# Performance work log

Measured on AMD Instinct MI355X. Metric: run time of the kernel, lower is better.

## Reference

```python
import jax, jax.numpy as jnp
import numpy as np
from jax import lax
jax.config.update("jax_enable_x64", True)

FNV_OFF = np.int64(-3750763034362895579)
FNV_PRIME = np.int64(4294967731)
I64_MAX = np.iinfo(np.int64).max
INF = np.float32(1e38)
CHUNK = 512  # cluster-chunk size for the cdist fallback


def _pack_key(b, c, vx, vy, vz):
    # five-word FNV-1a 64-bit hash with natural int64 wraparound
    h = jnp.full(b.shape, FNV_OFF, dtype=jnp.int64)
    for w in (b, c, vx, vy, vz):
        h = (h ^ w.astype(jnp.int64)) * FNV_PRIME
    return h


def _safe_norm(x):
    s = jnp.sum(x * x, axis=1)
    n = jnp.sqrt(jnp.where(s > 0, s, 1.0))
    return jnp.where(s > 0, n, 0.0)


def setup_inputs() -> dict:
    key = jax.random.key(0)
    k1, k2, k3, k4 = jax.random.split(key, 4)
    N = 65536
    grid = jax.random.randint(k1, (N, 3), 0, 400).astype(jnp.float32)
    batch_id = jnp.sort(jax.random.randint(k2, (N,), 0, 2).astype(jnp.int64))
    label = jax.random.randint(k3, (N,), 0, 8).astype(jnp.int64)
    pred_off = jax.random.normal(k4, (N, 3), dtype=jnp.float32)
    return {"pred_off": pred_off, "grid": grid, "label": label, "batch_id": batch_id,
            "base_grid": 16, "num_cls": 8, "num_batch": 2}


def _forward(pred_off, grid, label, batch_id, base_grid, num_cls, num_batch):
    N = grid.shape[0]
    grid_f = grid.astype(jnp.float32)
    vox = jnp.floor(grid_f / base_grid).astype(jnp.int64)  # [N,3]

    # voxel_grid: bucket by (batch, voxel) -> consecutive cluster ids via unique
    ckey = ((batch_id * 1024 + vox[:, 0]) * 1024 + vox[:, 1]) * 1024 + vox[:, 2]
    _, cluster = jnp.unique(ckey, return_inverse=True, size=N, fill_value=I64_MAX)
    cluster = cluster.reshape(-1)

    # cluster stats (segment scatter-reduce, num_segments = N upper bound)
    cnt = jax.ops.segment_sum(jnp.ones((N,), jnp.float32), cluster, num_segments=N)
    cl_center = jax.ops.segment_sum(grid_f, cluster, num_segments=N) / jnp.maximum(cnt, 1.0)[:, None]
    cl_batch = jax.ops.segment_min(batch_id, cluster, num_segments=N)
    cl_lbl_lo = jax.ops.segment_min(label, cluster, num_segments=N)
    cl_lbl_hi = jax.ops.segment_max(label, cluster, num_segments=N)
    cl_vox = jax.ops.segment_min(vox, cluster, num_segments=N)
    valid_cl = cnt > 0
    pure_cl = (cl_lbl_lo == cl_lbl_hi) & valid_cl
    pure_pt = pure_cl[cluster]

    # hash table of pure clusters, sorted by key (invalid -> sentinel, sorts last)
    pk_all = jnp.where(pure_cl, _pack_key(cl_batch, cl_lbl_lo, cl_vox[:, 0], cl_vox[:, 1], cl_vox[:, 2]), I64_MAX)
    order = jnp.argsort(pk_all)
    pk_sort = pk_all[order]
    pc_sort = cl_center[order]
    ok_sort = pure_cl[order]

    # per (batch,label) global centers
    key_bl = batch_id * num_cls + label
    nbl = num_batch * num_cls
    cnt_bl = jax.ops.segment_sum(jnp.ones((N,), jnp.float32), key_bl, num_segments=nbl)
    global_c = jax.ops.segment_sum(grid_f, key_bl, num_segments=nbl) / jnp.maximum(cnt_bl, 1.0)[:, None]
    step_sign = jnp.sign(global_c[key_bl] - cl_center[cluster]).astype(jnp.int64)  # [N,3]

    # +/-1 and +/-2 voxel hash lookup (steps 1 and K+1=2)
    def probe(step):
        cv = cl_vox[cluster] + step_sign * step
        ck = _pack_key(batch_id, label, cv[:, 0], cv[:, 1], cv[:, 2])
        idx = jnp.searchsorted(pk_sort, ck)
        idxc = jnp.minimum(idx, N - 1)
        hit = (idx < N) & ok_sort[idxc] & (pk_sort[idxc] == ck)
        return hit, pc_sort[idxc]

    hit1, t1 = probe(1)
    hit2, t2 = probe(2)
    hit_pt = hit1 | hit2
    tgt_c = jnp.where(hit1[:, None], t1, jnp.where(hit2[:, None], t2, grid_f))

    # fallback: nearest pure-cluster center with same (batch,label), chunked cdist+argmin
    miss = (~pure_pt) & (~hit_pt)
    code_y = key_bl
    code_x = jnp.where(pure_cl, cl_batch * num_cls + cl_lbl_lo, jnp.int64(-1))
    p2 = jnp.sum(grid_f * grid_f, axis=1)  # [N]

    def body(carry, i):
        best_d, best_c = carry
        c = lax.dynamic_slice_in_dim(cl_center, i * CHUNK, CHUNK)   # [S,3]
        cc = lax.dynamic_slice_in_dim(code_x, i * CHUNK, CHUNK)      # [S]
        d2 = p2[:, None] - 2.0 * (grid_f @ c.T) + jnp.sum(c * c, axis=1)[None, :]  # [N,S]
        d2 = jnp.where(cc[None, :] == code_y[:, None], d2, INF)
        j = jnp.argmin(d2, axis=1)
        dmin = jnp.take_along_axis(d2, j[:, None], axis=1)[:, 0]
        upd = dmin < best_d
        best_d = jnp.where(upd, dmin, best_d)
        best_c = jnp.where(upd[:, None], c[j], best_c)
        return (best_d, best_c), None

    nchunk = N // CHUNK
    (best_d, best_c), _ = lax.scan(body, (jnp.full((N,), INF, jnp.float32), grid_f), jnp.arange(nchunk))
    tgt_c = jnp.where((miss & (best_d < INF))[:, None], best_c, tgt_c)

    # loss: smooth-L1 on offsets below 99th-percentile magnitude + direction cosine loss
    tgt_off = tgt_c - grid_f
    mag = _safe_norm(tgt_off)
    thresh = jnp.quantile(mag, 0.99)
    m1 = mag <= thresh
    d = pred_off - tgt_off
    ad = jnp.abs(d)
    hub = jnp.where(ad < 1.0, 0.5 * d * d, ad - 0.5)
    n1 = jnp.sum(m1).astype(jnp.float32)
    loss_l1 = jnp.where(n1 > 0, jnp.sum(hub * m1[:, None]) / jnp.maximum(n1 * 3.0, 1.0), 0.0)

    md = (mag > 0) & m1
    eps = 1e-4
    pn = _safe_norm(pred_off)
    cos = jnp.sum(pred_off * tgt_off, axis=1) / jnp.maximum(pn * mag, eps)
    nmd = jnp.sum(md).astype(jnp.float32)
    loss_dir = jnp.where(nmd > 0, 1.0 - jnp.sum(cos * md) / jnp.maximum(nmd, 1.0), 0.0)
    return jnp.stack([loss_l1.astype(jnp.float32), loss_dir.astype(jnp.float32)])


def reference(pred_off, grid, label, batch_id, base_grid, num_cls, num_batch):
    return _forward(pred_off, grid, label, batch_id, base_grid, num_cls, num_batch)
```

## Files before the change

kernel.cpp:

```cpp
#include <hip/hip_runtime.h>
#include <climits>

#define VOXD 25
#define SLOT3 (VOXD*VOXD*VOXD)
#define SLOTS (2*SLOT3)
#define NCLS 8
#define NCODE 16
#define NBLK ((SLOTS + 255) / 256)
#define HB 2048
#define BPC 64
#define TILE 1024
#define CSTRIDE SLOT3

struct Scalars {
  double hub;
  double cosSum;
  int n1;
  int nmd;
  float thresh;
  int done;
  int done2;
};

__device__ __forceinline__ int voxslot(int b, int vx, int vy, int vz) {
  return ((b * VOXD + vx) * VOXD + vy) * VOXD + vz;
}

__device__ __forceinline__ int block_scan256(int v, int* ws) {
  int lane = threadIdx.x & 63, w = threadIdx.x >> 6;
  int s = v;
  #pragma unroll
  for (int off = 1; off < 64; off <<= 1) {
    int t = __shfl_up(s, off, 64);
    if (lane >= off) s += t;
  }
  if (lane == 63) ws[w] = s;
  __syncthreads();
  int add = 0;
  #pragma unroll
  for (int q = 0; q < 4; ++q) if (q < w) add += ws[q];
  __syncthreads();
  return s + add;
}

__global__ void k_scatter(const float* __restrict__ grid, const int* __restrict__ label,
                          const int* __restrict__ batch,
                          unsigned long long* vA, unsigned long long* vB, int* lmask,
                          int* blCnt, float* blSum, int n) {
  __shared__ int sCnt[NCODE];
  __shared__ float sSum[3 * NCODE];
  int tid = threadIdx.x;
  if (tid < NCODE) sCnt[tid] = 0;
  if (tid < 3 * NCODE) sSum[tid] = 0.f;
  __syncthreads();
  int i = blockIdx.x * blockDim.x + tid;
  if (i < n) {
    float gx = grid[3*i], gy = grid[3*i+1], gz = grid[3*i+2];
    int ix = (int)gx, iy = (int)gy, iz = (int)gz;
    int vx = (int)floorf(gx * (1.0f/16.0f));
    int vy = (int)floorf(gy * (1.0f/16.0f));
    int vz = (int)floorf(gz * (1.0f/16.0f));
    int b = batch[i], l = label[i];
    int s = voxslot(b, vx, vy, vz);
    atomicAdd(&vA[s], ((unsigned long long)(unsigned)ix << 32) | (unsigned)iy);
    atomicAdd(&vB[s], ((unsigned long long)(unsigned)iz << 24) | 1ULL);
    atomicOr(&lmask[s], 1 << l);
    int bl = b * NCLS + l;
    atomicAdd(&sCnt[bl], 1);
    atomicAdd(&sSum[3*bl], gx); atomicAdd(&sSum[3*bl+1], gy); atomicAdd(&sSum[3*bl+2], gz);
  }
  __syncthreads();
  if (tid < NCODE && sCnt[tid] != 0) atomicAdd(&blCnt[tid], sCnt[tid]);
  if (tid < 3 * NCODE && sSum[tid] != 0.f) atomicAdd(&blSum[tid], sSum[tid]);
}

__global__ void k_prep(const unsigned long long* vA, const unsigned long long* vB,
                       const int* lmask, float4* ctr, float4* pC, int* codeCnt) {
  __shared__ int lc[NCODE];
  __shared__ int lb[NCODE];
  int tid = threadIdx.x;
  if (tid < NCODE) lc[tid] = 0;
  __syncthreads();
  int s = blockIdx.x * 256 + tid;
  int code = -1, lpos = 0;
  float4 v = make_float4(0.f, 0.f, 0.f, __int_as_float(-2));
  if (s < SLOTS) {
    unsigned long long bq = vB[s];
    unsigned c = (unsigned)(bq & 0xFFFFFFULL);
    if (c > 0) {
      unsigned long long aq = vA[s];
      float fc = (float)c;
      float cx = __fdiv_rn((float)(unsigned)(aq >> 32), fc);
      float cy = __fdiv_rn((float)(unsigned)(aq & 0xFFFFFFFFULL), fc);
      float cz = __fdiv_rn((float)(unsigned)(bq >> 24), fc);
      int m = lmask[s];
      bool pure = (m & (m - 1)) == 0;
      int lbl = __ffs(m) - 1;
      v = make_float4(cx, cy, cz, __int_as_float(pure ? lbl : -1));
      if (pure) {
        code = (s / SLOT3) * NCLS + lbl;
        lpos = atomicAdd(&lc[code], 1);
      }
    }
    ctr[s] = v;
  }
  __syncthreads();
  if (tid < NCODE) lb[tid] = (lc[tid] > 0) ? atomicAdd(&codeCnt[tid], lc[tid]) : 0;
  __syncthreads();
  if (code >= 0) {
    int pos = code * CSTRIDE + lb[code] + lpos;
    pC[pos] = make_float4(v.x, v.y, v.z, __int_as_float(s));
  }
}

__global__ void k_targets(const float* __restrict__ grid, const int* __restrict__ label,
                          const int* __restrict__ batch,
                          const float4* __restrict__ ctr,
                          const int* __restrict__ blCnt, const float* __restrict__ blSum,
                          float* tgt, float* mag, int* ghist,
                          int* missPart, int* missCnt, int mstride, int n) {
  __shared__ int wCnt[4][NCODE];
  __shared__ int gBase[NCODE];
  __shared__ int h[HB];
  int tid = threadIdx.x, lane = tid & 63, w = tid >> 6;
  for (int t = tid; t < HB; t += 256) h[t] = 0;
  __syncthreads();
  int i = blockIdx.x * blockDim.x + tid;
  bool active = (i < n);
  bool miss = false;
  int mcode = -1;

  if (active) {
    float gx = grid[3*i], gy = grid[3*i+1], gz = grid[3*i+2];
    int vx = (int)floorf(gx * (1.0f/16.0f));
    int vy = (int)floorf(gy * (1.0f/16.0f));
    int vz = (int)floorf(gz * (1.0f/16.0f));
    int b = batch[i], l = label[i];
    int s = voxslot(b, vx, vy, vz);

    float4 own = ctr[s];
    bool purept = (__float_as_int(own.w) >= 0);

    int bl = b * NCLS + l;
    float fbc = (float)max(blCnt[bl], 1);
    float gcx = __fdiv_rn(blSum[3*bl],   fbc);
    float gcy = __fdiv_rn(blSum[3*bl+1], fbc);
    float gcz = __fdiv_rn(blSum[3*bl+2], fbc);

    float dx = __fsub_rn(gcx, own.x);
    float dy = __fsub_rn(gcy, own.y);
    float dz = __fsub_rn(gcz, own.z);
    int sgx = (dx > 0.f) ? 1 : ((dx < 0.f) ? -1 : 0);
    int sgy = (dy > 0.f) ? 1 : ((dy < 0.f) ? -1 : 0);
    int sgz = (dz > 0.f) ? 1 : ((dz < 0.f) ? -1 : 0);

    int ax1 = vx + sgx,     ay1 = vy + sgy,     az1 = vz + sgz;
    int ax2 = vx + 2 * sgx, ay2 = vy + 2 * sgy, az2 = vz + 2 * sgz;
    bool v1 = (unsigned)ax1 < (unsigned)VOXD && (unsigned)ay1 < (unsigned)VOXD &&
              (unsigned)az1 < (unsigned)VOXD;
    bool v2 = (unsigned)ax2 < (unsigned)VOXD && (unsigned)ay2 < (unsigned)VOXD &&
              (unsigned)az2 < (unsigned)VOXD;

    float4 q1 = make_float4(0.f, 0.f, 0.f, __int_as_float(-3));
    float4 q2 = q1;
    if (v1) q1 = ctr[voxslot(b, ax1, ay1, az1)];
    if (v2) q2 = ctr[voxslot(b, ax2, ay2, az2)];

    bool hit1 = v1 && (__float_as_int(q1.w) == l);
    bool hit2 = v2 && (__float_as_int(q2.w) == l);
    bool hit = hit1 || hit2;

    float tx = hit1 ? q1.x : (hit2 ? q2.x : gx);
    float ty = hit1 ? q1.y : (hit2 ? q2.y : gy);
    float tz = hit1 ? q1.z : (hit2 ? q2.z : gz);

    tgt[3*i] = tx; tgt[3*i+1] = ty; tgt[3*i+2] = tz;
    miss = (!purept && !hit);
    if (miss) {
      mcode = bl;
    } else {
      float tox = __fsub_rn(tx, gx), toy = __fsub_rn(ty, gy), toz = __fsub_rn(tz, gz);
      float ssq = __fadd_rn(__fadd_rn(__fmul_rn(tox,tox), __fmul_rn(toy,toy)),
                            __fmul_rn(toz,toz));
      float m = (ssq > 0.f) ? sqrtf(ssq) : 0.f;
      mag[i] = m;
      atomicAdd(&h[__float_as_uint(m) >> 21], 1);
    }
  }
  int myrank = 0;
  #pragma unroll
  for (int c = 0; c < NCODE; ++c) {
    unsigned long long mb = __ballot(mcode == c);
    if (lane == 0) wCnt[w][c] = __popcll(mb);
    if (mcode == c) myrank = __popcll(mb & ((1ULL << lane) - 1ULL));
  }
  __syncthreads();
  if (tid < NCODE) {
    int tot = wCnt[0][tid] + wCnt[1][tid] + wCnt[2][tid] + wCnt[3][tid];
    gBase[tid] = (tot > 0) ? atomicAdd(&missCnt[tid], tot) : 0;
  }
  __syncthreads();
  if (miss) {
    int base = gBase[mcode];
    for (int q = 0; q < 4; ++q) if (q < w) base += wCnt[q][mcode];
    missPart[mcode * mstride + base + myrank] = i;
  }
  for (int t = tid; t < HB; t += 256) {
    int c = h[t];
    if (c != 0) atomicAdd(&ghist[t], c);
  }
}

__global__ void __launch_bounds__(256) k_fallback(
    const float* __restrict__ grid,
    const float4* __restrict__ pC,
    const float4* __restrict__ ctr,
    const int* __restrict__ codeCnt,
    const int* __restrict__ missPart, const int* __restrict__ missCnt,
    float* tgt, float* mag, int* ghist, int mstride) {
  __shared__ float4 tile4[TILE];
  __shared__ int    stile[TILE];
  __shared__ unsigned long long bkeyw[4][64];
  __shared__ int h[HB];
  int tid = threadIdx.x, lane = tid & 63, w = tid >> 6;
  int c = blockIdx.x / BPC;
  int y = blockIdx.x % BPC;
  int mc = missCnt[c];
  if (y * 64 >= mc) return;
  int cc = codeCnt[c];
  int j0 = c * CSTRIDE;
  const int* mlist = missPart + c * mstride;

  for (int t = tid; t < HB; t += 256) h[t] = 0;
  __syncthreads();

  for (int t0 = y * 64; t0 < mc; t0 += BPC * 64) {
    int t = t0 + lane;
    bool valid = (t < mc);
    int idx = 0;
    float gx = 0.f, gy = 0.f, gz = 0.f, p2 = 0.f;
    if (valid) {
      idx = mlist[t];
      gx = grid[3*idx]; gy = grid[3*idx+1]; gz = grid[3*idx+2];
      p2 = __fadd_rn(__fadd_rn(__fmul_rn(gx,gx), __fmul_rn(gy,gy)),
                     __fmul_rn(gz,gz));
    }
    unsigned long long key = 0xFFFFFFFFFFFFFFFFULL;
    for (int tb = 0; tb < cc; tb += TILE) {
      int m = min(TILE, cc - tb);
      __syncthreads();
      for (int j = tid; j < m; j += 256) {
        float4 cl = pC[j0 + tb + j];
        float c2 = __fadd_rn(__fadd_rn(__fmul_rn(cl.x,cl.x), __fmul_rn(cl.y,cl.y)),
                             __fmul_rn(cl.z,cl.z));
        tile4[j] = make_float4(cl.x, cl.y, cl.z, c2);
        stile[j] = __float_as_int(cl.w);
      }
      __syncthreads();
      #pragma unroll 4
      for (int j = w; j < m; j += 4) {
        float4 cl = tile4[j];
        float dot = __fadd_rn(__fadd_rn(__fmul_rn(gx,cl.x), __fmul_rn(gy,cl.y)),
                              __fmul_rn(gz,cl.z));
        float d2 = __fadd_rn(__fsub_rn(p2, __fmul_rn(2.0f, dot)), cl.w);
        unsigned fb = __float_as_uint(d2);
        fb = (fb >> 31) ? ~fb : (fb | 0x80000000u);
        unsigned long long k2 = ((unsigned long long)fb << 32) | (unsigned)stile[j];
        if (k2 < key) key = k2;
      }
    }
    bkeyw[w][lane] = key;
    __syncthreads();
    if (w == 0 && valid) {
      unsigned long long k0 = bkeyw[0][lane];
      unsigned long long k1 = bkeyw[1][lane];
      unsigned long long k2_ = bkeyw[2][lane];
      unsigned long long k3 = bkeyw[3][lane];
      unsigned long long kk = k0 < k1 ? k0 : k1;
      unsigned long long kh = k2_ < k3 ? k2_ : k3;
      if (kh < kk) kk = kh;
      float mv = 0.f;
      if (cc > 0) {
        int slot = (int)(unsigned)(kk & 0xFFFFFFFFULL);
        float4 cl = ctr[slot];
        tgt[3*idx] = cl.x; tgt[3*idx+1] = cl.y; tgt[3*idx+2] = cl.z;
        float tox = __fsub_rn(cl.x, gx), toy = __fsub_rn(cl.y, gy),
              toz = __fsub_rn(cl.z, gz);
        float ssq = __fadd_rn(__fadd_rn(__fmul_rn(tox,tox), __fmul_rn(toy,toy)),
                              __fmul_rn(toz,toz));
        mv = (ssq > 0.f) ? sqrtf(ssq) : 0.f;
      }
      mag[idx] = mv;
      atomicAdd(&h[__float_as_uint(mv) >> 21], 1);
    }
    __syncthreads();
  }

  for (int t = tid; t < HB; t += 256) {
    int cv = h[t];
    if (cv != 0) atomicAdd(&ghist[t], cv);
  }
}

__global__ void __launch_bounds__(256) k_loss_sel(
    const float* __restrict__ pred, const float* __restrict__ grid,
    const float* __restrict__ tgt, const float* __restrict__ mag,
    const int* __restrict__ ghist, uint2* defer, int* uCnt,
    Scalars* sc, float* out, int n, int nblocks, int r0, int r1, double tfrac) {
  __shared__ int h[HB];
  __shared__ int h2[HB];
  __shared__ int ws[4];
  __shared__ int s_misc[8];
  __shared__ double shH[256];
  __shared__ double shC[256];
  __shared__ int shN[256];
  __shared__ int shM[256];
  __shared__ int sLast;
  __shared__ float sTh;
  int tid = threadIdx.x, lane = tid & 63;

  int base8 = tid * 8;
  {
    int cbin[8];
    int s = 0;
    #pragma unroll
    for (int k = 0; k < 8; ++k) { cbin[k] = ghist[base8 + k]; s += cbin[k]; }
    int incl = block_scan256(s, ws);
    int lo = incl - s;
    if (r0 >= lo && r0 < lo + s) {
      int acc = lo;
      #pragma unroll
      for (int k = 0; k < 8; ++k) {
        if (r0 < acc + cbin[k]) { s_misc[0] = base8 + k; s_misc[1] = r0 - acc; break; }
        acc += cbin[k];
      }
    }
    if (r1 >= lo && r1 < lo + s) {
      int acc = lo;
      #pragma unroll
      for (int k = 0; k < 8; ++k) {
        if (r1 < acc + cbin[k]) { s_misc[2] = base8 + k; s_misc[3] = r1 - acc; break; }
        acc += cbin[k];
      }
    }
  }
  __syncthreads();
  int binA = s_misc[0], rA = s_misc[1], binB = s_misc[2], rB = s_misc[3];

  int i = blockIdx.x * 256 + tid;
  double hub = 0.0, cs = 0.0;
  int c1 = 0, cmd = 0;
  bool dfr = false;
  unsigned bits = 0;
  if (i < n) {
    float m = mag[i];
    bits = __float_as_uint(m);
    int cb = (int)(bits >> 21);
    if (cb == binA || cb == binB) {
      dfr = true;
    } else if (cb < binA) {
      c1 = 1;
      float tox = __fsub_rn(tgt[3*i],   grid[3*i]);
      float toy = __fsub_rn(tgt[3*i+1], grid[3*i+1]);
      float toz = __fsub_rn(tgt[3*i+2], grid[3*i+2]);
      float px = pred[3*i], py = pred[3*i+1], pz = pred[3*i+2];
      float d0 = __fsub_rn(px, tox), d1 = __fsub_rn(py, toy), d2 = __fsub_rn(pz, toz);
      float a0 = fabsf(d0), a1 = fabsf(d1), a2 = fabsf(d2);
      float h0 = (a0 < 1.f) ? __fmul_rn(__fmul_rn(0.5f, d0), d0) : __fsub_rn(a0, 0.5f);
      float h1 = (a1 < 1.f) ? __fmul_rn(__fmul_rn(0.5f, d1), d1) : __fsub_rn(a1, 0.5f);
      float h2v = (a2 < 1.f) ? __fmul_rn(__fmul_rn(0.5f, d2), d2) : __fsub_rn(a2, 0.5f);
      hub = (double)h0 + (double)h1 + (double)h2v;
      if (m > 0.f) {
        cmd = 1;
        float ps = __fadd_rn(__fadd_rn(__fmul_rn(px,px), __fmul_rn(py,py)), __fmul_rn(pz,pz));
        float pn = (ps > 0.f) ? sqrtf(ps) : 0.f;
        float dotp = __fadd_rn(__fadd_rn(__fmul_rn(px,tox), __fmul_rn(py,toy)),
                               __fmul_rn(pz,toz));
        float den = fmaxf(__fmul_rn(pn, m), 1e-4f);
        cs = (double)__fdiv_rn(dotp, den);
      }
    }
  }
  {
    unsigned long long mb = __ballot(dfr);
    int mcp = __popcll(mb);
    int bs = 0;
    if (lane == 0 && mcp > 0) bs = atomicAdd(uCnt, mcp);
    bs = __shfl(bs, 0, 64);
    if (dfr) defer[bs + __popcll(mb & ((1ULL << lane) - 1ULL))] =
        make_uint2(bits, (unsigned)i);
  }
  shH[tid] = hub; shC[tid] = cs; shN[tid] = c1; shM[tid] = cmd;
  __syncthreads();
  for (int off = 128; off > 0; off >>= 1) {
    if (tid < off) {
      shH[tid] += shH[tid+off];
      shC[tid] += shC[tid+off];
      shN[tid] += shN[tid+off];
      shM[tid] += shM[tid+off];
    }
    __syncthreads();
  }
  if (tid == 0) {
    atomicAdd(&sc->hub, shH[0]);
    atomicAdd(&sc->cosSum, shC[0]);
    atomicAdd(&sc->n1, shN[0]);
    atomicAdd(&sc->nmd, shM[0]);
    __threadfence();
    int d = atomicAdd(&sc->done2, 1);
    sLast = (d == nblocks - 1) ? 1 : 0;
  }
  __syncthreads();
  if (!sLast) return;
  __threadfence();

  int U = atomicAdd(uCnt, 0);

  for (int t = tid; t < HB; t += 256) { h[t] = 0; h2[t] = 0; }
  __syncthreads();
  for (int t = tid; t < U; t += 256) {
    unsigned v = defer[t].x;
    int cb = (int)(v >> 21);
    if (cb == binA) atomicAdd(&h[(v >> 10) & 0x7FF], 1);
    if (cb == binB) atomicAdd(&h2[(v >> 10) & 0x7FF], 1);
  }
  __syncthreads();
  {
    int a8[8], sA = 0;
    #pragma unroll
    for (int k = 0; k < 8; ++k) { a8[k] = h[base8 + k]; sA += a8[k]; }
    int inclA = block_scan256(sA, ws);
    int accA = inclA - sA;
    #pragma unroll
    for (int k = 0; k < 8; ++k) {
      if (rA >= accA && rA < accA + a8[k]) { s_misc[4] = base8 + k; s_misc[5] = rA - accA; }
      accA += a8[k];
    }
    int b8[8], sB = 0;
    #pragma unroll
    for (int k = 0; k < 8; ++k) { b8[k] = h2[base8 + k]; sB += b8[k]; }
    int inclB = block_scan256(sB, ws);
    int accB = inclB - sB;
    #pragma unroll
    for (int k = 0; k < 8; ++k) {
      if (rB >= accB && rB < accB + b8[k]) { s_misc[6] = base8 + k; s_misc[7] = rB - accB; }
      accB += b8[k];
    }
  }
  __syncthreads();
  int subA = s_misc[4], subRA = s_misc[5], subB = s_misc[6], subRB = s_misc[7];

  for (int t = tid; t < 1024; t += 256) { h[t] = 0; h2[t] = 0; }
  __syncthreads();
  for (int t = tid; t < U; t += 256) {
    unsigned v = defer[t].x;
    int cb = (int)(v >> 21);
    if (cb == binA && (int)((v >> 10) & 0x7FF) == subA) atomicAdd(&h[v & 0x3FF], 1);
    if (cb == binB && (int)((v >> 10) & 0x7FF) == subB) atomicAdd(&h2[v & 0x3FF], 1);
  }
  __syncthreads();
  {
    int base4 = tid * 4;
    int la[4], sA = 0;
    #pragma unroll
    for (int k = 0; k < 4; ++k) { la[k] = h[base4 + k]; sA += la[k]; }
    int inclA = block_scan256(sA, ws);
    int accA = inclA - sA;
    #pragma unroll
    for (int k = 0; k < 4; ++k) {
      if (subRA >= accA && subRA < accA + la[k]) s_misc[0] = base4 + k;
      accA += la[k];
    }
    int lb4[4], sB = 0;
    #pragma unroll
    for (int k = 0; k < 4; ++k) { lb4[k] = h2[base4 + k]; sB += lb4[k]; }
    int inclB = block_scan256(sB, ws);
    int accB = inclB - sB;
    #pragma unroll
    for (int k = 0; k < 4; ++k) {
      if (subRB >= accB && subRB < accB + lb4[k]) s_misc[1] = base4 + k;
      accB += lb4[k];
    }
  }
  __syncthreads();
  if (tid == 0) {
    unsigned va = ((unsigned)binA << 21) | ((unsigned)subA << 10) | (unsigned)s_misc[0];
    unsigned vb = ((unsigned)binB << 21) | ((unsigned)subB << 10) | (unsigned)s_misc[1];
    double a = (double)__uint_as_float(va);
    double b = (double)__uint_as_float(vb);
    double th = (tfrac >= 0.5) ? (b - (b - a) * (1.0 - tfrac)) : (a + (b - a) * tfrac);
    sc->thresh = (float)th;
    sTh = (float)th;
  }
  __syncthreads();
  float th = sTh;

  double hub2 = 0.0, cs2 = 0.0;
  int c12 = 0, cmd2 = 0;
  for (int t = tid; t < U; t += 256) {
    uint2 e = defer[t];
    float m = __uint_as_float(e.x);
    if (m <= th) {
      int idx = (int)e.y;
      c12 += 1;
      float tox = __fsub_rn(tgt[3*idx],   grid[3*idx]);
      float toy = __fsub_rn(tgt[3*idx+1], grid[3*idx+1]);
      float toz = __fsub_rn(tgt[3*idx+2], grid[3*idx+2]);
      float px = pred[3*idx], py = pred[3*idx+1], pz = pred[3*idx+2];
      float d0 = __fsub_rn(px, tox), d1 = __fsub_rn(py, toy), d2 = __fsub_rn(pz, toz);
      float a0 = fabsf(d0), a1 = fabsf(d1), a2 = fabsf(d2);
      float h0 = (a0 < 1.f) ? __fmul_rn(__fmul_rn(0.5f, d0), d0) : __fsub_rn(a0, 0.5f);
      float h1 = (a1 < 1.f) ? __fmul_rn(__fmul_rn(0.5f, d1), d1) : __fsub_rn(a1, 0.5f);
      float h2v = (a2 < 1.f) ? __fmul_rn(__fmul_rn(0.5f, d2), d2) : __fsub_rn(a2, 0.5f);
      hub2 += (double)h0 + (double)h1 + (double)h2v;
      if (m > 0.f) {
        cmd2 += 1;
        float ps = __fadd_rn(__fadd_rn(__fmul_rn(px,px), __fmul_rn(py,py)), __fmul_rn(pz,pz));
        float pn = (ps > 0.f) ? sqrtf(ps) : 0.f;
        float dotp = __fadd_rn(__fadd_rn(__fmul_rn(px,tox), __fmul_rn(py,toy)),
                               __fmul_rn(pz,toz));
        float den = fmaxf(__fmul_rn(pn, m), 1e-4f);
        cs2 += (double)__fdiv_rn(dotp, den);
      }
    }
  }
  shH[tid] = hub2; shC[tid] = cs2; shN[tid] = c12; shM[tid] = cmd2;
  __syncthreads();
  for (int off = 128; off > 0; off >>= 1) {
    if (tid < off) {
      shH[tid] += shH[tid+off];
      shC[tid] += shC[tid+off];
      shN[tid] += shN[tid+off];
      shM[tid] += shM[tid+off];
    }
    __syncthreads();
  }
  if (tid == 0) {
    double th_hub = atomicAdd(&sc->hub, 0.0) + shH[0];
    double th_cos = atomicAdd(&sc->cosSum, 0.0) + shC[0];
    int n1 = atomicAdd(&sc->n1, 0) + shN[0];
    int nmd = atomicAdd(&sc->nmd, 0) + shM[0];
    double l1 = (n1 > 0) ? th_hub / fmax((double)n1 * 3.0, 1.0) : 0.0;
    double ld = (nmd > 0) ? (1.0 - th_cos / fmax((double)nmd, 1.0)) : 0.0;
    out[0] = (float)l1;
    out[1] = (float)ld;
  }
}

extern "C" void kernel_launch(void* const* d_in, const int* in_sizes, int n_in,
                              void* d_out, int out_size, void* d_ws, size_t ws_size,
                              hipStream_t stream) {
  const float* pred  = (const float*)d_in[0];
  const float* grid  = (const float*)d_in[1];
  const int*   label = (const int*)d_in[2];
  const int*   batch = (const int*)d_in[3];
  int n = in_sizes[2];
  int mstride = n / 4;

  char* p = (char*)d_ws;
  auto take = [&](size_t bytes) -> char* {
    char* r = p;
    p += (bytes + 255) & ~(size_t)255;
    return r;
  };
  char* zbase = p;
  unsigned long long* vA = (unsigned long long*)take((size_t)SLOTS*8);
  unsigned long long* vB = (unsigned long long*)take((size_t)SLOTS*8);
  int*    lmask    = (int*)   take((size_t)SLOTS*4);
  int*    codeCnt  = (int*)   take(NCODE*4);
  int*    missCnt  = (int*)   take(NCODE*4);
  int*    blCnt    = (int*)   take(16*4);
  float*  blSum    = (float*) take(48*4);
  int*    ghist    = (int*)   take((size_t)HB*4);
  int*    uCnt     = (int*)   take(4);
  Scalars* sc      = (Scalars*)take(sizeof(Scalars));
  size_t zbytes = (size_t)(p - zbase);
  float4* ctr      = (float4*)take((size_t)SLOTS*16);
  float4* pC       = (float4*)take((size_t)NCODE*CSTRIDE*16);
  float*  tgt      = (float*) take((size_t)n*3*4);
  float*  mag      = (float*) take((size_t)n*4);
  int*    missPart = (int*)   take((size_t)NCODE*mstride*4);
  uint2*  defer    = (uint2*) take((size_t)n*8);

  int nb = (n + 255) / 256;
  int nfb = NCODE * BPC;

  double vi = 0.99 * (double)(n - 1);
  int r0 = (int)vi;
  int r1 = r0 + 1; if (r1 > n - 1) r1 = n - 1;
  double tfrac = vi - (double)r0;

  hipMemsetAsync(zbase, 0, zbytes, stream);
  k_scatter<<<nb, 256, 0, stream>>>(grid, label, batch, vA, vB, lmask,
                                    blCnt, blSum, n);
  k_prep<<<NBLK, 256, 0, stream>>>(vA, vB, lmask, ctr, pC, codeCnt);
  k_targets<<<nb, 256, 0, stream>>>(grid, label, batch, ctr, blCnt, blSum,
                                    tgt, mag, ghist, missPart, missCnt, mstride, n);
  k_fallback<<<nfb, 256, 0, stream>>>(grid, pC, ctr, codeCnt,
                                      missPart, missCnt, tgt, mag, ghist, mstride);
  k_loss_sel<<<nb, 256, 0, stream>>>(pred, grid, tgt, mag, ghist, defer, uCnt,
                                     sc, (float*)d_out, n, nb, r0, r1, tfrac);
}
```

Measured before the change: 142.3 us.

## Move boundary-bin histogramming and loss precompute into parallel phase of selection kernel

The quantile-selection kernel now builds the second-level histogram for boundary-bin elements in every block, merging it through global atomics, instead of having the last block rescan the deferred list. Deferred elements store their precomputed huber and cosine terms, so the last block no longer gathers pred, tgt and grid per element. The first-level scan over the deferred bits uses vectorised uint4 loads. The aim is to shorten the serial single-block tail, at the cost of extra global atomics and 16 more bytes written per deferred element.

```diff
diff --git a/kernel.cpp b/kernel.cpp
--- a/kernel.cpp
+++ b/kernel.cpp
@@ -305,7 +305,8 @@
 __global__ void __launch_bounds__(256) k_loss_sel(
     const float* __restrict__ pred, const float* __restrict__ grid,
     const float* __restrict__ tgt, const float* __restrict__ mag,
-    const int* __restrict__ ghist, uint2* defer, int* uCnt,
+    const int* __restrict__ ghist, int* gh2A, int* gh2B,
+    unsigned* dBits, double2* dHC, int* uCnt,
     Scalars* sc, float* out, int n, int nblocks, int r0, int r1, double tfrac) {
   __shared__ int h[HB];
   __shared__ int h2[HB];
@@ -347,19 +348,21 @@
   __syncthreads();
   int binA = s_misc[0], rA = s_misc[1], binB = s_misc[2], rB = s_misc[3];
 
+  for (int t = tid; t < HB; t += 256) { h[t] = 0; h2[t] = 0; }
+  __syncthreads();
+
   int i = blockIdx.x * 256 + tid;
   double hub = 0.0, cs = 0.0;
   int c1 = 0, cmd = 0;
   bool dfr = false;
   unsigned bits = 0;
+  double dhub = 0.0, dcs = 0.0;
   if (i < n) {
     float m = mag[i];
     bits = __float_as_uint(m);
     int cb = (int)(bits >> 21);
-    if (cb == binA || cb == binB) {
-      dfr = true;
-    } else if (cb < binA) {
-      c1 = 1;
+    bool boundary = (cb == binA || cb == binB);
+    if (boundary || cb < binA) {
       float tox = __fsub_rn(tgt[3*i],   grid[3*i]);
       float toy = __fsub_rn(tgt[3*i+1], grid[3*i+1]);
       float toz = __fsub_rn(tgt[3*i+2], grid[3*i+2]);
@@ -369,15 +372,25 @@
       float h0 = (a0 < 1.f) ? __fmul_rn(__fmul_rn(0.5f, d0), d0) : __fsub_rn(a0, 0.5f);
       float h1 = (a1 < 1.f) ? __fmul_rn(__fmul_rn(0.5f, d1), d1) : __fsub_rn(a1, 0.5f);
       float h2v = (a2 < 1.f) ? __fmul_rn(__fmul_rn(0.5f, d2), d2) : __fsub_rn(a2, 0.5f);
-      hub = (double)h0 + (double)h1 + (double)h2v;
+      double hubv = (double)h0 + (double)h1 + (double)h2v;
+      double csv = 0.0;
       if (m > 0.f) {
-        cmd = 1;
         float ps = __fadd_rn(__fadd_rn(__fmul_rn(px,px), __fmul_rn(py,py)), __fmul_rn(pz,pz));
         float pn = (ps > 0.f) ? sqrtf(ps) : 0.f;
         float dotp = __fadd_rn(__fadd_rn(__fmul_rn(px,tox), __fmul_rn(py,toy)),
                                __fmul_rn(pz,toz));
         float den = fmaxf(__fmul_rn(pn, m), 1e-4f);
-        cs = (double)__fdiv_rn(dotp, den);
+        csv = (double)__fdiv_rn(dotp, den);
+      }
+      if (boundary) {
+        dfr = true;
+        dhub = hubv; dcs = csv;
+        if (cb == binA) atomicAdd(&h[(bits >> 10) & 0x7FF], 1);
+        if (cb == binB) atomicAdd(&h2[(bits >> 10) & 0x7FF], 1);
+      } else {
+        c1 = 1;
+        hub = hubv;
+        if (m > 0.f) { cmd = 1; cs = csv; }
       }
     }
   }
@@ -387,9 +400,20 @@
     int bs = 0;
     if (lane == 0 && mcp > 0) bs = atomicAdd(uCnt, mcp);
     bs = __shfl(bs, 0, 64);
-    if (dfr) defer[bs + __popcll(mb & ((1ULL << lane) - 1ULL))] =
-        make_uint2(bits, (unsigned)i);
-  }
+    if (dfr) {
+      int pos = bs + __popcll(mb & ((1ULL << lane) - 1ULL));
+      dBits[pos] = bits;
+      dHC[pos] = make_double2(dhub, dcs);
+    }
+  }
+  __syncthreads();
+  for (int t = tid; t < HB; t += 256) {
+    int a = h[t];
+    if (a != 0) atomicAdd(&gh2A[t], a);
+    int b = h2[t];
+    if (b != 0) atomicAdd(&gh2B[t], b);
+  }
+
   shH[tid] = hub; shC[tid] = cs; shN[tid] = c1; shM[tid] = cmd;
   __syncthreads();
   for (int off = 128; off > 0; off >>= 1) {
@@ -416,19 +440,10 @@
 
   int U = atomicAdd(uCnt, 0);
 
-  for (int t = tid; t < HB; t += 256) { h[t] = 0; h2[t] = 0; }
-  __syncthreads();
-  for (int t = tid; t < U; t += 256) {
-    unsigned v = defer[t].x;
-    int cb = (int)(v >> 21);
-    if (cb == binA) atomicAdd(&h[(v >> 10) & 0x7FF], 1);
-    if (cb == binB) atomicAdd(&h2[(v >> 10) & 0x7FF], 1);
-  }
-  __syncthreads();
   {
     int a8[8], sA = 0;
     #pragma unroll
-    for (int k = 0; k < 8; ++k) { a8[k] = h[base8 + k]; sA += a8[k]; }
+    for (int k = 0; k < 8; ++k) { a8[k] = gh2A[base8 + k]; sA += a8[k]; }
     int inclA = block_scan256(sA, ws);
     int accA = inclA - sA;
     #pragma unroll
@@ -438,7 +453,7 @@
     }
     int b8[8], sB = 0;
     #pragma unroll
-    for (int k = 0; k < 8; ++k) { b8[k] = h2[base8 + k]; sB += b8[k]; }
+    for (int k = 0; k < 8; ++k) { b8[k] = gh2B[base8 + k]; sB += b8[k]; }
     int inclB = block_scan256(sB, ws);
     int accB = inclB - sB;
     #pragma unroll
@@ -452,11 +467,26 @@
 
   for (int t = tid; t < 1024; t += 256) { h[t] = 0; h2[t] = 0; }
   __syncthreads();
-  for (int t = tid; t < U; t += 256) {
-    unsigned v = defer[t].x;
-    int cb = (int)(v >> 21);
-    if (cb == binA && (int)((v >> 10) & 0x7FF) == subA) atomicAdd(&h[v & 0x3FF], 1);
-    if (cb == binB && (int)((v >> 10) & 0x7FF) == subB) atomicAdd(&h2[v & 0x3FF], 1);
+  {
+    const uint4* b4 = (const uint4*)dBits;
+    int nv = U >> 2;
+    for (int v = tid; v < nv; v += 256) {
+      uint4 u = b4[v];
+      unsigned bb[4] = { u.x, u.y, u.z, u.w };
+      #pragma unroll
+      for (int k = 0; k < 4; ++k) {
+        unsigned b0 = bb[k];
+        int cb = (int)(b0 >> 21);
+        if (cb == binA && (int)((b0 >> 10) & 0x7FF) == subA) atomicAdd(&h[b0 & 0x3FF], 1);
+        if (cb == binB && (int)((b0 >> 10) & 0x7FF) == subB) atomicAdd(&h2[b0 & 0x3FF], 1);
+      }
+    }
+    for (int t = (nv << 2) + tid; t < U; t += 256) {
+      unsigned b0 = dBits[t];
+      int cb = (int)(b0 >> 21);
+      if (cb == binA && (int)((b0 >> 10) & 0x7FF) == subA) atomicAdd(&h[b0 & 0x3FF], 1);
+      if (cb == binB && (int)((b0 >> 10) & 0x7FF) == subB) atomicAdd(&h2[b0 & 0x3FF], 1);
+    }
   }
   __syncthreads();
   {
@@ -498,30 +528,13 @@
   double hub2 = 0.0, cs2 = 0.0;
   int c12 = 0, cmd2 = 0;
   for (int t = tid; t < U; t += 256) {
-    uint2 e = defer[t];
-    float m = __uint_as_float(e.x);
+    unsigned v = dBits[t];
+    float m = __uint_as_float(v);
+    double2 hc = dHC[t];
     if (m <= th) {
-      int idx = (int)e.y;
       c12 += 1;
-      float tox = __fsub_rn(tgt[3*idx],   grid[3*idx]);
-      float toy = __fsub_rn(tgt[3*idx+1], grid[3*idx+1]);
-      float toz = __fsub_rn(tgt[3*idx+2], grid[3*idx+2]);
-      float px = pred[3*idx], py = pred[3*idx+1], pz = pred[3*idx+2];
-      float d0 = __fsub_rn(px, tox), d1 = __fsub_rn(py, toy), d2 = __fsub_rn(pz, toz);
-      float a0 = fabsf(d0), a1 = fabsf(d1), a2 = fabsf(d2);
-      float h0 = (a0 < 1.f) ? __fmul_rn(__fmul_rn(0.5f, d0), d0) : __fsub_rn(a0, 0.5f);
-      float h1 = (a1 < 1.f) ? __fmul_rn(__fmul_rn(0.5f, d1), d1) : __fsub_rn(a1, 0.5f);
-      float h2v = (a2 < 1.f) ? __fmul_rn(__fmul_rn(0.5f, d2), d2) : __fsub_rn(a2, 0.5f);
-      hub2 += (double)h0 + (double)h1 + (double)h2v;
-      if (m > 0.f) {
-        cmd2 += 1;
-        float ps = __fadd_rn(__fadd_rn(__fmul_rn(px,px), __fmul_rn(py,py)), __fmul_rn(pz,pz));
-        float pn = (ps > 0.f) ? sqrtf(ps) : 0.f;
-        float dotp = __fadd_rn(__fadd_rn(__fmul_rn(px,tox), __fmul_rn(py,toy)),
-                               __fmul_rn(pz,toz));
-        float den = fmaxf(__fmul_rn(pn, m), 1e-4f);
-        cs2 += (double)__fdiv_rn(dotp, den);
-      }
+      hub2 += hc.x;
+      if (m > 0.f) { cmd2 += 1; cs2 += hc.y; }
     }
   }
   shH[tid] = hub2; shC[tid] = cs2; shN[tid] = c12; shM[tid] = cmd2;
@@ -572,6 +585,8 @@
   int*    blCnt    = (int*)   take(16*4);
   float*  blSum    = (float*) take(48*4);
   int*    ghist    = (int*)   take((size_t)HB*4);
+  int*    gh2A     = (int*)   take((size_t)HB*4);
+  int*    gh2B     = (int*)   take((size_t)HB*4);
   int*    uCnt     = (int*)   take(4);
   Scalars* sc      = (Scalars*)take(sizeof(Scalars));
   size_t zbytes = (size_t)(p - zbase);
@@ -580,7 +595,8 @@
   float*  tgt      = (float*) take((size_t)n*3*4);
   float*  mag      = (float*) take((size_t)n*4);
   int*    missPart = (int*)   take((size_t)NCODE*mstride*4);
-  uint2*  defer    = (uint2*) take((size_t)n*8);
+  unsigned* dBits  = (unsigned*)take((size_t)n*4);
+  double2*  dHC    = (double2*) take((size_t)n*16);
 
   int nb = (n + 255) / 256;
   int nfb = NCODE * BPC;
@@ -598,6 +614,7 @@
                                     tgt, mag, ghist, missPart, missCnt, mstride, n);
   k_fallback<<<nfb, 256, 0, stream>>>(grid, pC, ctr, codeCnt,
                                       missPart, missCnt, tgt, mag, ghist, mstride);
-  k_loss_sel<<<nb, 256, 0, stream>>>(pred, grid, tgt, mag, ghist, defer, uCnt,
-                                     sc, (float*)d_out, n, nb, r0, r1, tfrac);
-}
+  k_loss_sel<<<nb, 256, 0, stream>>>(pred, grid, tgt, mag, ghist, gh2A, gh2B,
+                                     dBits, dHC, uCnt, sc, (float*)d_out,
+                                     n, nb, r0, r1, tfrac);
+}
```

Result: faster. 138.3 us (-2.8%).
